# Optimization experiments

Hardware: AMD Instinct MI355X
Metric: run time of the kernel (lower is better)

## Reference

```python
import jax, jax.numpy as jnp
import numpy as np

N_TEST, N_TRAIN, D = 16384, 8192, 64


def setup_inputs() -> dict:
    key = jax.random.key(0)
    k1, k2, k3 = jax.random.split(key, 3)
    test_X = jax.random.normal(k1, (N_TEST, D), dtype=jnp.float32)
    train_X = jax.random.normal(k2, (N_TRAIN, D), dtype=jnp.float32)
    alphas = jax.random.normal(k3, (N_TRAIN, 1), dtype=jnp.float32)
    lengthscale = jnp.ones((1,), dtype=jnp.float32)
    return {"test_X": test_X, "train_X": train_X, "alphas": alphas, "lengthscale": lengthscale}


def reference(test_X, train_X, alphas, lengthscale):
    # gpytorch RBFKernel: scale inputs by lengthscale, squared dist, exp(-0.5 * d2)
    xs = test_X / lengthscale    # [n_test, d]
    ts = train_X / lengthscale   # [n_train, d]
    sq = (jnp.sum(xs * xs, axis=-1, keepdims=True)
          - 2.0 * (xs @ ts.T)
          + jnp.sum(ts * ts, axis=-1)[None, :])  # [n_test, n_train]
    K = jnp.exp(-0.5 * jnp.maximum(sq, 0.0))
    return K @ alphas  # [n_test, 1]
```

## Files before the change

### kernel.cpp

```cpp
#include <hip/hip_runtime.h>

#define NTEST  16384
#define NTRAIN 8192
#define DIM    64
#define NCOLSPLIT 16
#define WPB    8

typedef _Float16 f16x8  __attribute__((ext_vector_type(8)));
typedef float    f32x16 __attribute__((ext_vector_type(16)));

#define LOG2E 1.4426950408889634f

#define GLOAD_LDS16(gsrc, ldst)                                                     \
    __builtin_amdgcn_global_load_lds(                                               \
        (const __attribute__((address_space(1))) unsigned int*)(gsrc),              \
        (__attribute__((address_space(3))) unsigned int*)(ldst), 16, 0, 0)

__global__ __launch_bounds__(256) void krr_prep(
    const float* __restrict__ test_X, const float* __restrict__ train_X,
    const float* __restrict__ alphas, const float* __restrict__ lengthscale,
    _Float16* __restrict__ A_hi, _Float16* __restrict__ B_hi,
    float* __restrict__ nx2, float* __restrict__ wt)
{
    int gwave = (blockIdx.x * 256 + threadIdx.x) >> 6;
    int lane  = threadIdx.x & 63;
    bool is_test = gwave < NTEST;
    int row = is_test ? gwave : gwave - NTEST;
    const float* src = is_test ? test_X : train_X;

    float x = src[(size_t)row * DIM + lane];
    _Float16 h = (_Float16)x;

    if (is_test) {
        A_hi[(size_t)row * DIM + lane] = h;
    } else {
        int t  = row >> 5, lr = row & 31;
        int kk = lane >> 4, hi = (lane >> 3) & 1, e = lane & 7;
        size_t dst = (size_t)t * 2048 + (size_t)kk * 512 + (size_t)(hi * 32 + lr) * 8 + e;
        B_hi[dst] = h;
    }

    float s = x * x;
    s += __shfl_xor(s, 1);  s += __shfl_xor(s, 2);  s += __shfl_xor(s, 4);
    s += __shfl_xor(s, 8);  s += __shfl_xor(s, 16); s += __shfl_xor(s, 32);
    if (lane == 0) {
        float ls   = lengthscale[0];
        float inv2 = 1.0f / (ls * ls);
        float cn   = -0.5f * inv2 * LOG2E;
        if (is_test) nx2[row] = s * cn;
        else         wt[row]  = alphas[row] * __builtin_amdgcn_exp2f(cn * s);
    }
}

__global__ __launch_bounds__(512) void krr_mfma(
    const _Float16* __restrict__ A_hi, const _Float16* __restrict__ B_hi,
    const float* __restrict__ nx2, const float* __restrict__ wt,
    const float* __restrict__ lengthscale, float* __restrict__ out)
{
    alignas(16) __shared__ _Float16 Bs[8 * 2048];
    __shared__ float wts[512];

    const int tid   = threadIdx.x;
    const int lane  = tid & 63;
    const int wave  = tid >> 6;
    const int rbase = blockIdx.x * 256 + wave * 32;
    const int cb    = blockIdx.y;

    const float ls   = lengthscale[0];
    const float inv2 = 1.0f / (ls * ls);
    const float s1   = inv2 * LOG2E;

    wts[tid] = wt[cb * 512 + tid];

    const int arow = rbase + (lane & 31);
    const int koff = (lane >> 5) * 8;

    f16x8 ah[4];
    #pragma unroll
    for (int kk = 0; kk < 4; ++kk)
        ah[kk] = *reinterpret_cast<const f16x8*>(A_hi + (size_t)arow * DIM + kk * 16 + koff);

    float nxc[16];
    #pragma unroll
    for (int r = 0; r < 16; ++r) {
        int row = (r & 3) + 8 * (r >> 2) + 4 * (lane >> 5);
        nxc[r] = nx2[rbase + row];
    }

    float acc[16];
    #pragma unroll
    for (int r = 0; r < 16; ++r) acc[r] = 0.0f;

    for (int p = 0; p < 2; ++p) {
        if (p) __syncthreads();

        {
            const _Float16* gt = B_hi + ((size_t)cb * 16 + p * 8 + wave) * 2048
                               + (size_t)lane * 8;
            _Float16* lt0 = &Bs[(size_t)wave * 2048];
            GLOAD_LDS16(gt,        lt0);
            GLOAD_LDS16(gt + 512,  lt0 + 512);
            GLOAD_LDS16(gt + 1024, lt0 + 1024);
            GLOAD_LDS16(gt + 1536, lt0 + 1536);
        }
        __syncthreads();

        #pragma unroll 1
        for (int lt = 0; lt < 8; lt += 2) {
            const _Float16* pA = &Bs[(size_t)lt * 2048 + (size_t)lane * 8];
            const _Float16* pB = pA + 2048;
            f16x8 bhA[4], bhB[4];
            #pragma unroll
            for (int kk = 0; kk < 4; ++kk) {
                bhA[kk] = *reinterpret_cast<const f16x8*>(pA + kk * 512);
                bhB[kk] = *reinterpret_cast<const f16x8*>(pB + kk * 512);
            }
            const int wtb = (p * 8 + lt) * 32 + (lane & 31);
            const float wA = wts[wtb];
            const float wB = wts[wtb + 32];

            f32x16 CA = {};
            f32x16 CB = {};
            #pragma unroll
            for (int kk = 0; kk < 4; ++kk) {
                CA = __builtin_amdgcn_mfma_f32_32x32x16_f16(ah[kk], bhA[kk], CA, 0, 0, 0);
                CB = __builtin_amdgcn_mfma_f32_32x32x16_f16(ah[kk], bhB[kk], CB, 0, 0, 0);
            }

            #pragma unroll
            for (int r = 0; r < 16; ++r) {
                float argA = fmaf(CA[r], s1, nxc[r]);
                float argB = fmaf(CB[r], s1, nxc[r]);
                acc[r] = fmaf(__builtin_amdgcn_exp2f(argA), wA, acc[r]);
                acc[r] = fmaf(__builtin_amdgcn_exp2f(argB), wB, acc[r]);
            }
        }
    }

    #pragma unroll
    for (int r = 0; r < 16; ++r) {
        float v = acc[r];
        v += __shfl_xor(v, 1);  v += __shfl_xor(v, 2);  v += __shfl_xor(v, 4);
        v += __shfl_xor(v, 8);  v += __shfl_xor(v, 16);
        if ((lane & 31) == 0) {
            int row = (r & 3) + 8 * (r >> 2) + 4 * (lane >> 5);
            atomicAdd(&out[rbase + row], v);
        }
    }
}

#define TCHUNK 512
#define NCHUNK (NTRAIN / TCHUNK)
__global__ __launch_bounds__(256, 4) void krr_main(
    const float* __restrict__ test_X, const float* __restrict__ train_X,
    const float* __restrict__ alphas, const float* __restrict__ lengthscale,
    float* __restrict__ out)
{
    __shared__ float nt_lds[TCHUNK];
    __shared__ float al_lds[TCHUNK];
    const int tid = threadIdx.x;
    const int i   = blockIdx.x * 256 + tid;
    const int j0  = blockIdx.y * TCHUNK;
    const float ls   = lengthscale[0];
    const float inv2 = 1.0f / (ls * ls);
    for (int jj = tid; jj < TCHUNK; jj += 256) {
        const float4* tr = reinterpret_cast<const float4*>(train_X + (size_t)(j0 + jj) * DIM);
        float s = 0.f;
        #pragma unroll
        for (int k = 0; k < DIM / 4; ++k) {
            float4 t = tr[k];
            s += t.x * t.x + t.y * t.y + t.z * t.z + t.w * t.w;
        }
        nt_lds[jj] = s * inv2;
        al_lds[jj] = alphas[j0 + jj];
    }
    __syncthreads();
    float xr[DIM]; float nxv = 0.f;
    {
        const float4* xp = reinterpret_cast<const float4*>(test_X + (size_t)i * DIM);
        #pragma unroll
        for (int k = 0; k < DIM / 4; ++k) {
            float4 v = xp[k];
            xr[4*k+0] = v.x; xr[4*k+1] = v.y; xr[4*k+2] = v.z; xr[4*k+3] = v.w;
            nxv += v.x*v.x + v.y*v.y + v.z*v.z + v.w*v.w;
        }
        nxv *= inv2;
        #pragma unroll
        for (int k = 0; k < DIM; ++k) xr[k] *= inv2;
    }
    float acc = 0.f;
    for (int jj = 0; jj < TCHUNK; ++jj) {
        const float* trow = train_X + (size_t)(j0 + jj) * DIM;
        float d0 = 0.f, d1 = 0.f, d2 = 0.f, d3 = 0.f;
        #pragma unroll
        for (int k4 = 0; k4 < DIM / 4; ++k4) {
            float4 t = reinterpret_cast<const float4*>(trow)[k4];
            d0 = fmaf(xr[4*k4+0], t.x, d0);
            d1 = fmaf(xr[4*k4+1], t.y, d1);
            d2 = fmaf(xr[4*k4+2], t.z, d2);
            d3 = fmaf(xr[4*k4+3], t.w, d3);
        }
        float dot = (d0 + d1) + (d2 + d3);
        float sq  = nxv + nt_lds[jj] - 2.0f * dot;
        sq = fmaxf(sq, 0.0f);
        acc = fmaf(__expf(-0.5f * sq), al_lds[jj], acc);
    }
    atomicAdd(&out[i], acc);
}

extern "C" void kernel_launch(void* const* d_in, const int* in_sizes, int n_in,
                              void* d_out, int out_size, void* d_ws, size_t ws_size,
                              hipStream_t stream) {
    const float* test_X      = (const float*)d_in[0];
    const float* train_X     = (const float*)d_in[1];
    const float* alphas      = (const float*)d_in[2];
    const float* lengthscale = (const float*)d_in[3];
    float* out = (float*)d_out;

    hipMemsetAsync(out, 0, NTEST * sizeof(float), stream);

    const size_t need = (size_t)(NTEST + NTRAIN) * DIM * sizeof(_Float16)
                      + (NTEST + NTRAIN) * sizeof(float);
    if (ws_size >= need) {
        _Float16* A_hi = (_Float16*)d_ws;
        _Float16* B_hi = A_hi + (size_t)NTEST * DIM;
        float*    nx2  = (float*)(B_hi + (size_t)NTRAIN * DIM);
        float*    wtp  = nx2 + NTEST;

        krr_prep<<<(NTEST + NTRAIN) / 4, 256, 0, stream>>>(
            test_X, train_X, alphas, lengthscale, A_hi, B_hi, nx2, wtp);

        dim3 grid(NTEST / 256, NCOLSPLIT);
        krr_mfma<<<grid, 64 * WPB, 0, stream>>>(A_hi, B_hi, nx2, wtp,
                                                lengthscale, out);
    } else {
        dim3 grid(NTEST / 256, NCHUNK);
        krr_main<<<grid, 256, 0, stream>>>(test_X, train_X, alphas, lengthscale, out);
    }
}
```

Measured before the change: 45.52 us.

## Double-buffer B tiles in LDS to overlap global loads with MFMA compute

The single 8-tile LDS staging buffer is split into two 4-tile buffers, and the column block is processed as four units. The global-to-LDS load of the next unit is issued before computing on the current one, which is meant to hide load latency behind the MFMA and exp2 work. The inner loop is also fully unrolled. The compiler may insert conservative vmcnt waits before the LDS reads, which would remove the overlap, and the extra barriers add synchronisation cost.

```diff
diff --git a/kernel.cpp b/kernel.cpp
--- a/kernel.cpp
+++ b/kernel.cpp
@@ -57,7 +57,8 @@
     const float* __restrict__ nx2, const float* __restrict__ wt,
     const float* __restrict__ lengthscale, float* __restrict__ out)
 {
-    alignas(16) __shared__ _Float16 Bs[8 * 2048];
+    alignas(16) __shared__ _Float16 BsA[4 * 2048];
+    alignas(16) __shared__ _Float16 BsB[4 * 2048];
     __shared__ float wts[512];
 
     const int tid   = threadIdx.x;
@@ -91,23 +92,19 @@
     #pragma unroll
     for (int r = 0; r < 16; ++r) acc[r] = 0.0f;
 
-    for (int p = 0; p < 2; ++p) {
-        if (p) __syncthreads();
-
-        {
-            const _Float16* gt = B_hi + ((size_t)cb * 16 + p * 8 + wave) * 2048
-                               + (size_t)lane * 8;
-            _Float16* lt0 = &Bs[(size_t)wave * 2048];
-            GLOAD_LDS16(gt,        lt0);
-            GLOAD_LDS16(gt + 512,  lt0 + 512);
-            GLOAD_LDS16(gt + 1024, lt0 + 1024);
-            GLOAD_LDS16(gt + 1536, lt0 + 1536);
-        }
-        __syncthreads();
-
-        #pragma unroll 1
-        for (int lt = 0; lt < 8; lt += 2) {
-            const _Float16* pA = &Bs[(size_t)lt * 2048 + (size_t)lane * 8];
+    #define STAGE_UNIT(u, buf)                                                  \
+        {                                                                       \
+            const _Float16* g = B_hi + ((size_t)cb * 16 + (u) * 4) * 2048       \
+                              + (size_t)wave * 1024 + (size_t)lane * 8;         \
+            _Float16* l = (buf) + (size_t)wave * 1024;                          \
+            GLOAD_LDS16(g,       l);                                            \
+            GLOAD_LDS16(g + 512, l + 512);                                      \
+        }
+
+    auto compute4 = [&](const _Float16* buf, int u) {
+        #pragma unroll
+        for (int lt = 0; lt < 4; lt += 2) {
+            const _Float16* pA = buf + (size_t)lt * 2048 + (size_t)lane * 8;
             const _Float16* pB = pA + 2048;
             f16x8 bhA[4], bhB[4];
             #pragma unroll
@@ -115,7 +112,7 @@
                 bhA[kk] = *reinterpret_cast<const f16x8*>(pA + kk * 512);
                 bhB[kk] = *reinterpret_cast<const f16x8*>(pB + kk * 512);
             }
-            const int wtb = (p * 8 + lt) * 32 + (lane & 31);
+            const int wtb = u * 128 + lt * 32 + (lane & 31);
             const float wA = wts[wtb];
             const float wB = wts[wtb + 32];
 
@@ -135,7 +132,22 @@
                 acc[r] = fmaf(__builtin_amdgcn_exp2f(argB), wB, acc[r]);
             }
         }
-    }
+    };
+
+    STAGE_UNIT(0, BsA);
+    __syncthreads();
+    STAGE_UNIT(1, BsB);
+    compute4(BsA, 0);
+    __syncthreads();
+    STAGE_UNIT(2, BsA);
+    compute4(BsB, 1);
+    __syncthreads();
+    STAGE_UNIT(3, BsB);
+    compute4(BsA, 2);
+    __syncthreads();
+    compute4(BsB, 3);
+
+    #undef STAGE_UNIT
 
     #pragma unroll
     for (int r = 0; r < 16; ++r) {
```

Result: slower. 98.77 us (+117.0%).
